# Performance work log

Measured on AMD Instinct MI355X. Metric: run time of the kernel, lower is better.

Reference implementation:

```python
import jax, jax.numpy as jnp
import numpy as np

H = 32       # num query heads
KV = 8       # num kv heads
HD = 128     # head dim
G = H // KV  # groups


def setup_inputs() -> dict:
    key = jax.random.key(0)
    ks = jax.random.split(key, 7)
    B, S, P, D = 2, 2048, 1024, 4096
    s = 1.0 / np.sqrt(D)
    return {
        "x": jax.random.normal(ks[0], (B, S, D), jnp.float32),
        "past_k": jax.random.normal(ks[1], (B, P, KV, HD), jnp.float32),
        "past_v": jax.random.normal(ks[2], (B, P, KV, HD), jnp.float32),
        "Wq": jax.random.normal(ks[3], (D, H * HD), jnp.float32) * s,
        "Wk": jax.random.normal(ks[4], (D, KV * HD), jnp.float32) * s,
        "Wv": jax.random.normal(ks[5], (D, KV * HD), jnp.float32) * s,
        "Wo": jax.random.normal(ks[6], (D, D), jnp.float32) * s,
    }


def reference(x, past_k, past_v, Wq, Wk, Wv, Wo):
    B, S, D = x.shape
    q = (x @ Wq).reshape(B, S, H, HD)    # [B,S,H,hd]
    k = (x @ Wk).reshape(B, S, KV, HD)
    v = (x @ Wv).reshape(B, S, KV, HD)
    # KV-cache append (cache slice [:, :end])
    k_full = jnp.concatenate([past_k, k], axis=1)  # [B,T,KV,hd]
    v_full = jnp.concatenate([past_v, v], axis=1)
    T = k_full.shape[1]
    # repeat_interleave over head dim -> each kv head serves G query heads
    k_rep = jnp.repeat(k_full, G, axis=2)  # [B,T,H,hd]
    v_rep = jnp.repeat(v_full, G, axis=2)
    scale = 1.0 / np.sqrt(HD)
    scores = jnp.einsum('bshd,bthd->bhst', q, k_rep) * scale  # [B,H,S,T]
    # causal mask with cache offset: query i attends to j <= (T - S) + i
    allowed = (jnp.arange(S)[:, None] + (T - S)) >= jnp.arange(T)[None, :]
    scores = jnp.where(allowed[None, None], scores, jnp.float32(-jnp.inf))
    attn = jax.nn.softmax(scores, axis=-1)
    out = jnp.einsum('bhst,bthd->bshd', attn, v_rep).reshape(B, S, D)
    return out @ Wo
```

## Files before the change

### kernel.cpp

```cpp
#include <hip/hip_runtime.h>

typedef __bf16 bf16x8 __attribute__((ext_vector_type(8)));
typedef float f32x4 __attribute__((ext_vector_type(4)));
using gptr_t = const __attribute__((address_space(1))) void*;
using sptr_t = __attribute__((address_space(3))) void*;

#define B_ 2
#define S_ 2048
#define D_ 4096
#define H_ 32
#define KV_ 8
#define G_ 4
#define HD_ 128
#define P_ 1024
#define T_ 3072

__device__ inline bf16x8 cvt8(const float4 a, const float4 b) {
  bf16x8 r;
  r[0] = (__bf16)a.x; r[1] = (__bf16)a.y; r[2] = (__bf16)a.z; r[3] = (__bf16)a.w;
  r[4] = (__bf16)b.x; r[5] = (__bf16)b.y; r[6] = (__bf16)b.z; r[7] = (__bf16)b.w;
  return r;
}

__global__ __launch_bounds__(256) void cvt_f32_bf16(const float* __restrict__ in,
                                                    __bf16* __restrict__ out) {
  const long i = ((long)blockIdx.x * 256 + threadIdx.x) * 8;
  float4 a = *(const float4*)(in + i);
  float4 b = *(const float4*)(in + i + 4);
  *(bf16x8*)(out + i) = cvt8(a, b);
}

__global__ __launch_bounds__(256) void transpose2d(const float* __restrict__ in,
                                                   __bf16* __restrict__ out,
                                                   int R, int C) {
  __shared__ float tl[32][33];
  const int tx = threadIdx.x, ty = threadIdx.y;
  const int c0 = blockIdx.x * 32, r0 = blockIdx.y * 32;
#pragma unroll
  for (int i = 0; i < 4; ++i)
    tl[ty + i * 8][tx] = in[(long)(r0 + ty + i * 8) * C + c0 + tx];
  __syncthreads();
#pragma unroll
  for (int i = 0; i < 4; ++i)
    out[(long)(c0 + ty + i * 8) * R + r0 + tx] = (__bf16)tl[tx][ty + i * 8];
}

__global__ __launch_bounds__(256) void build_vt(const float* __restrict__ past_v,
                                                const __bf16* __restrict__ vn,
                                                __bf16* __restrict__ vt) {
  __shared__ float tl[32][33];
  const int tx = threadIdx.x, ty = threadIdx.y;
  const int j0 = blockIdx.x * 32, hd0 = blockIdx.y * 32;
  const int b = blockIdx.z >> 3, kvh = blockIdx.z & 7;
#pragma unroll
  for (int i = 0; i < 4; ++i) {
    const int j = j0 + ty + i * 8;
    float val = (j < P_)
        ? past_v[((long)((b * P_ + j) * KV_ + kvh)) * HD_ + hd0 + tx]
        : (float)vn[((long)((b * S_ + (j - P_)) * KV_ + kvh)) * HD_ + hd0 + tx];
    tl[ty + i * 8][tx] = val;
  }
  __syncthreads();
#pragma unroll
  for (int i = 0; i < 4; ++i)
    vt[((long)((b * KV_ + kvh) * HD_ + hd0 + ty + i * 8)) * T_ + j0 + tx] =
        (__bf16)tl[tx][ty + i * 8];
}

template <typename OutT>
__global__ __launch_bounds__(256, 3) void gemm_bt(const __bf16* __restrict__ A,
                                                  const __bf16* __restrict__ Bt,
                                                  OutT* __restrict__ C,
                                                  int M, int N, int K) {
  __shared__ __align__(16) __bf16 As[128][32];
  __shared__ __align__(16) __bf16 Bs[128][32];
  const int t = threadIdx.x;
  const int lane = t & 63, wave = t >> 6;
  const int wm = (wave >> 1) * 64, wn = (wave & 1) * 64;
  const int l15 = lane & 15, quad = lane >> 4;
  const long m0 = (long)blockIdx.y * 128, n0 = (long)blockIdx.x * 128;

  const int srow = wave * 32 + (lane >> 2);
  const int scol = (lane & 3) * 8;
  const __bf16* Ap = A + (m0 + srow) * K + scol;
  const __bf16* Bp = Bt + (n0 + srow) * K + scol;
  const long rstep = 16L * K;
  sptr_t ldsA0 = (sptr_t)&As[wave * 32][0];
  sptr_t ldsA1 = (sptr_t)&As[wave * 32 + 16][0];
  sptr_t ldsB0 = (sptr_t)&Bs[wave * 32][0];
  sptr_t ldsB1 = (sptr_t)&Bs[wave * 32 + 16][0];

  f32x4 acc[4][4];
#pragma unroll
  for (int i = 0; i < 4; ++i)
#pragma unroll
    for (int j = 0; j < 4; ++j)
#pragma unroll
      for (int e = 0; e < 4; ++e) acc[i][j][e] = 0.0f;

  const int nk = K >> 5;
  for (int kt = 0; kt < nk; ++kt) {
    __syncthreads();
    __builtin_amdgcn_global_load_lds((gptr_t)(Ap + kt * 32), ldsA0, 16, 0, 0);
    __builtin_amdgcn_global_load_lds((gptr_t)(Ap + rstep + kt * 32), ldsA1, 16, 0, 0);
    __builtin_amdgcn_global_load_lds((gptr_t)(Bp + kt * 32), ldsB0, 16, 0, 0);
    __builtin_amdgcn_global_load_lds((gptr_t)(Bp + rstep + kt * 32), ldsB1, 16, 0, 0);
    __syncthreads();
    bf16x8 aF[4], bF[4];
#pragma unroll
    for (int i = 0; i < 4; ++i)
      aF[i] = *(const bf16x8*)(&As[wm + i * 16 + l15][quad * 8]);
#pragma unroll
    for (int i = 0; i < 4; ++i)
      bF[i] = *(const bf16x8*)(&Bs[wn + i * 16 + l15][quad * 8]);
#pragma unroll
    for (int i = 0; i < 4; ++i)
#pragma unroll
      for (int j = 0; j < 4; ++j)
        acc[i][j] = __builtin_amdgcn_mfma_f32_16x16x32_bf16(aF[i], bF[j],
                                                            acc[i][j], 0, 0, 0);
  }

#pragma unroll
  for (int i = 0; i < 4; ++i) {
    const long r0 = m0 + wm + i * 16 + quad * 4;
#pragma unroll
    for (int j = 0; j < 4; ++j) {
      const long col = n0 + wn + j * 16 + l15;
#pragma unroll
      for (int r = 0; r < 4; ++r)
        C[(r0 + r) * N + col] = (OutT)acc[i][j][r];
    }
  }
}

__global__ __launch_bounds__(256, 2) void attn_kernel(
    __bf16* qio,
    const float* __restrict__ pk,
    const __bf16* __restrict__ kn,
    const __bf16* __restrict__ vt) {
  __shared__ __align__(16) __bf16 Ks[64][136];
  __shared__ __align__(16) __bf16 Vs[128][72];
  __shared__ __align__(16) __bf16 Ps[4][32][72];
  const int t = threadIdx.x;
  const int lane = t & 63, w = t >> 6;
  const int l15 = lane & 15, quad = lane >> 4;
  const int s0 = blockIdx.x * 128;
  const int h = blockIdx.y, b = blockIdx.z;
  const int kvh = h >> 2;

  bf16x8 aQ[2][4];
#pragma unroll
  for (int mi = 0; mi < 2; ++mi) {
    const int qrow = s0 + w * 32 + mi * 16 + l15;
    const __bf16* qp = qio + ((long)((b * S_ + qrow) * H_ + h)) * HD_ + quad * 8;
#pragma unroll
    for (int kt = 0; kt < 4; ++kt) aQ[mi][kt] = *(const bf16x8*)(qp + kt * 32);
  }

  f32x4 O[2][8];
#pragma unroll
  for (int mi = 0; mi < 2; ++mi)
#pragma unroll
    for (int f = 0; f < 8; ++f)
#pragma unroll
      for (int e = 0; e < 4; ++e) O[mi][f][e] = 0.0f;
  float m_r[2][4], l_r[2][4];
#pragma unroll
  for (int mi = 0; mi < 2; ++mi)
#pragma unroll
    for (int r = 0; r < 4; ++r) { m_r[mi][r] = -__builtin_inff(); l_r[mi][r] = 0.0f; }

  bf16x8 ones;
#pragma unroll
  for (int e = 0; e < 8; ++e) ones[e] = (__bf16)1.0f;

  const float C2 = 1.4426950408889634f * 0.08838834764831845f;
  const int ntiles = (P_ + s0 + 128) / 64;
  const int wave_last_key = P_ + s0 + w * 32 + 31;
  const int wave_min_bound = P_ + s0 + w * 32;

  for (int tile = 0; tile < ntiles; ++tile) {
    const int j0 = tile * 64;
    __syncthreads();
#pragma unroll
    for (int p = 0; p < 4; ++p) {
      const int li = p * 256 + t;
      const int key = li >> 4, ch = (li & 15) * 8;
      const int j = j0 + key;
      bf16x8 kv;
      if (j < P_) {
        const float* src = pk + ((long)((b * P_ + j) * KV_ + kvh)) * HD_ + ch;
        kv = cvt8(*(const float4*)src, *(const float4*)(src + 4));
      } else {
        kv = *(const bf16x8*)(kn + ((long)((b * S_ + (j - P_)) * KV_ + kvh)) * HD_ + ch);
      }
      *(bf16x8*)(&Ks[key][ch]) = kv;
    }
#pragma unroll
    for (int p = 0; p < 4; ++p) {
      const int li = p * 256 + t;
      const int hd = li >> 3, k8 = (li & 7) * 8;
      *(bf16x8*)(&Vs[hd][k8]) =
          *(const bf16x8*)(vt + ((long)((b * KV_ + kvh) * HD_ + hd)) * T_ + j0 + k8);
    }
    __syncthreads();

    if (j0 > wave_last_key) continue;

    f32x4 sc[2][4];
#pragma unroll
    for (int mi = 0; mi < 2; ++mi)
#pragma unroll
      for (int kf = 0; kf < 4; ++kf)
#pragma unroll
        for (int e = 0; e < 4; ++e) sc[mi][kf][e] = 0.0f;
#pragma unroll
    for (int kf = 0; kf < 4; ++kf) {
#pragma unroll
      for (int kt = 0; kt < 4; ++kt) {
        bf16x8 bk = *(const bf16x8*)(&Ks[kf * 16 + l15][kt * 32 + quad * 8]);
        sc[0][kf] = __builtin_amdgcn_mfma_f32_16x16x32_bf16(aQ[0][kt], bk, sc[0][kf], 0, 0, 0);
        sc[1][kf] = __builtin_amdgcn_mfma_f32_16x16x32_bf16(aQ[1][kt], bk, sc[1][kf], 0, 0, 0);
      }
    }

    const bool need_mask = (j0 + 63 > wave_min_bound);
    float alpha[2][4];
#pragma unroll
    for (int mi = 0; mi < 2; ++mi) {
#pragma unroll
      for (int r = 0; r < 4; ++r) {
        float v0 = sc[mi][0][r], v1 = sc[mi][1][r];
        float v2 = sc[mi][2][r], v3 = sc[mi][3][r];
        if (need_mask) {
          const int bound = P_ + s0 + w * 32 + mi * 16 + quad * 4 + r;
          v0 = (j0 + l15 <= bound) ? v0 : -__builtin_inff();
          v1 = (j0 + 16 + l15 <= bound) ? v1 : -__builtin_inff();
          v2 = (j0 + 32 + l15 <= bound) ? v2 : -__builtin_inff();
          v3 = (j0 + 48 + l15 <= bound) ? v3 : -__builtin_inff();
        }
        float mt = fmaxf(fmaxf(v0, v1), fmaxf(v2, v3));
        mt = fmaxf(mt, __shfl_xor(mt, 1));
        mt = fmaxf(mt, __shfl_xor(mt, 2));
        mt = fmaxf(mt, __shfl_xor(mt, 4));
        mt = fmaxf(mt, __shfl_xor(mt, 8));
        const float mn = fmaxf(m_r[mi][r], mt);
        const float p0 = exp2f((v0 - mn) * C2);
        const float p1 = exp2f((v1 - mn) * C2);
        const float p2 = exp2f((v2 - mn) * C2);
        const float p3 = exp2f((v3 - mn) * C2);
        alpha[mi][r] = exp2f((m_r[mi][r] - mn) * C2);
        m_r[mi][r] = mn;
        const int row = mi * 16 + quad * 4 + r;
        Ps[w][row][l15] = (__bf16)p0;
        Ps[w][row][16 + l15] = (__bf16)p1;
        Ps[w][row][32 + l15] = (__bf16)p2;
        Ps[w][row][48 + l15] = (__bf16)p3;
      }
    }
#pragma unroll
    for (int mi = 0; mi < 2; ++mi)
#pragma unroll
      for (int f = 0; f < 8; ++f)
#pragma unroll
        for (int r = 0; r < 4; ++r) O[mi][f][r] *= alpha[mi][r];

    f32x4 sums[2];
#pragma unroll
    for (int e = 0; e < 4; ++e) { sums[0][e] = 0.0f; sums[1][e] = 0.0f; }
#pragma unroll
    for (int kf2 = 0; kf2 < 2; ++kf2) {
      bf16x8 aP0 = *(const bf16x8*)(&Ps[w][l15][kf2 * 32 + quad * 8]);
      bf16x8 aP1 = *(const bf16x8*)(&Ps[w][16 + l15][kf2 * 32 + quad * 8]);
      sums[0] = __builtin_amdgcn_mfma_f32_16x16x32_bf16(aP0, ones, sums[0], 0, 0, 0);
      sums[1] = __builtin_amdgcn_mfma_f32_16x16x32_bf16(aP1, ones, sums[1], 0, 0, 0);
#pragma unroll
      for (int f = 0; f < 8; ++f) {
        bf16x8 bV = *(const bf16x8*)(&Vs[f * 16 + l15][kf2 * 32 + quad * 8]);
        O[0][f] = __builtin_amdgcn_mfma_f32_16x16x32_bf16(aP0, bV, O[0][f], 0, 0, 0);
        O[1][f] = __builtin_amdgcn_mfma_f32_16x16x32_bf16(aP1, bV, O[1][f], 0, 0, 0);
      }
    }
#pragma unroll
    for (int mi = 0; mi < 2; ++mi)
#pragma unroll
      for (int r = 0; r < 4; ++r)
        l_r[mi][r] = l_r[mi][r] * alpha[mi][r] + sums[mi][r];
  }

#pragma unroll
  for (int mi = 0; mi < 2; ++mi) {
#pragma unroll
    for (int r = 0; r < 4; ++r) {
      const float inv = 1.0f / l_r[mi][r];
      const long row =
          (long)((b * S_ + s0 + w * 32 + mi * 16 + quad * 4 + r) * H_ + h);
#pragma unroll
      for (int f = 0; f < 8; ++f)
        qio[row * HD_ + f * 16 + l15] = (__bf16)(O[mi][f][r] * inv);
    }
  }
}

extern "C" void kernel_launch(void* const* d_in, const int* in_sizes, int n_in,
                              void* d_out, int out_size, void* d_ws, size_t ws_size,
                              hipStream_t stream) {
  const float* x  = (const float*)d_in[0];
  const float* pk = (const float*)d_in[1];
  const float* pv = (const float*)d_in[2];
  const float* Wq = (const float*)d_in[3];
  const float* Wk = (const float*)d_in[4];
  const float* Wv = (const float*)d_in[5];
  const float* Wo = (const float*)d_in[6];
  float* out = (float*)d_out;
  char* ws = (char*)d_ws;
  __bf16* wt = (__bf16*)(ws);
  __bf16* q  = (__bf16*)(ws + (size_t)33554432);
  __bf16* kn = (__bf16*)(ws + (size_t)67108864);
  __bf16* vn = (__bf16*)(ws + (size_t)75497472);
  __bf16* xb = (__bf16*)(ws + (size_t)83886080);
  __bf16* vt = (__bf16*)(ws + (size_t)83886080);

  dim3 tb(32, 8);
  cvt_f32_bf16<<<8192, 256, 0, stream>>>(x, xb);
  transpose2d<<<dim3(128, 128), tb, 0, stream>>>(Wq, wt, D_, D_);
  gemm_bt<__bf16><<<dim3(32, 32), 256, 0, stream>>>(xb, wt, q, B_ * S_, D_, D_);
  transpose2d<<<dim3(32, 128), tb, 0, stream>>>(Wk, wt, D_, KV_ * HD_);
  gemm_bt<__bf16><<<dim3(8, 32), 256, 0, stream>>>(xb, wt, kn, B_ * S_, KV_ * HD_, D_);
  transpose2d<<<dim3(32, 128), tb, 0, stream>>>(Wv, wt, D_, KV_ * HD_);
  gemm_bt<__bf16><<<dim3(8, 32), 256, 0, stream>>>(xb, wt, vn, B_ * S_, KV_ * HD_, D_);
  build_vt<<<dim3(96, 4, 16), tb, 0, stream>>>(pv, vn, vt);
  attn_kernel<<<dim3(16, 32, 2), 256, 0, stream>>>(q, pk, kn, vt);
  transpose2d<<<dim3(128, 128), tb, 0, stream>>>(Wo, wt, D_, D_);
  gemm_bt<float><<<dim3(32, 32), 256, 0, stream>>>(q, wt, out, B_ * S_, D_, D_);
}
```

Before: 1.219 ms.

## Fuse K/V projections, prebuild bf16 K cache, async LDS loads with swizzle

Fuses the K and V projection GEMMs into a single N=2048 GEMM and adds a pre-pass that builds a contiguous bf16 K cache per (batch, kv-head), so the attention kernel no longer converts fp32 past_k on the fly. The attention kernel now loads K and V tiles directly global-to-LDS with global_load_lds using an XOR-swizzled layout instead of padded arrays. It also reorders the grid so the longest causal query blocks are scheduled first, and raises the occupancy hint to 3. The costs are an extra build kernel and more workspace traffic, plus the risk that the swizzle addressing is wrong.

New measurement: 1.436 ms. 17.8% more time.

```diff
diff --git a/kernel.cpp b/kernel.cpp
--- a/kernel.cpp
+++ b/kernel.cpp
@@ -45,8 +45,27 @@
     out[(long)(c0 + ty + i * 8) * R + r0 + tx] = (__bf16)tl[tx][ty + i * 8];
 }
 
+__global__ __launch_bounds__(256) void build_kc(const float* __restrict__ pk,
+                                                const __bf16* __restrict__ kv,
+                                                __bf16* __restrict__ kc) {
+  const int i = blockIdx.x * 256 + threadIdx.x;
+  const int hd0 = (i & 15) * 8;
+  const int row = i >> 4;
+  const int j = row % T_;
+  const int bk = row / T_;
+  const int b = bk >> 3, kvh = bk & 7;
+  bf16x8 v;
+  if (j < P_) {
+    const float* src = pk + ((long)((b * P_ + j) * KV_ + kvh)) * HD_ + hd0;
+    v = cvt8(*(const float4*)src, *(const float4*)(src + 4));
+  } else {
+    v = *(const bf16x8*)(kv + (long)(b * S_ + (j - P_)) * 2048 + kvh * HD_ + hd0);
+  }
+  *(bf16x8*)(kc + (long)row * HD_ + hd0) = v;
+}
+
 __global__ __launch_bounds__(256) void build_vt(const float* __restrict__ past_v,
-                                                const __bf16* __restrict__ vn,
+                                                const __bf16* __restrict__ kv,
                                                 __bf16* __restrict__ vt) {
   __shared__ float tl[32][33];
   const int tx = threadIdx.x, ty = threadIdx.y;
@@ -57,7 +76,7 @@
     const int j = j0 + ty + i * 8;
     float val = (j < P_)
         ? past_v[((long)((b * P_ + j) * KV_ + kvh)) * HD_ + hd0 + tx]
-        : (float)vn[((long)((b * S_ + (j - P_)) * KV_ + kvh)) * HD_ + hd0 + tx];
+        : (float)kv[(long)(b * S_ + (j - P_)) * 2048 + 1024 + kvh * HD_ + hd0 + tx];
     tl[ty + i * 8][tx] = val;
   }
   __syncthreads();
@@ -134,19 +153,18 @@
   }
 }
 
-__global__ __launch_bounds__(256, 2) void attn_kernel(
+__global__ __launch_bounds__(256, 3) void attn_kernel(
     __bf16* qio,
-    const float* __restrict__ pk,
-    const __bf16* __restrict__ kn,
+    const __bf16* __restrict__ kc,
     const __bf16* __restrict__ vt) {
-  __shared__ __align__(16) __bf16 Ks[64][136];
-  __shared__ __align__(16) __bf16 Vs[128][72];
+  __shared__ __align__(16) __bf16 Ks[64][128];
+  __shared__ __align__(16) __bf16 Vs[128][64];
   __shared__ __align__(16) __bf16 Ps[4][32][72];
   const int t = threadIdx.x;
   const int lane = t & 63, w = t >> 6;
   const int l15 = lane & 15, quad = lane >> 4;
-  const int s0 = blockIdx.x * 128;
-  const int h = blockIdx.y, b = blockIdx.z;
+  const int s0 = (15 - blockIdx.z) * 128;
+  const int h = blockIdx.x, b = blockIdx.y;
   const int kvh = h >> 2;
 
   bf16x8 aQ[2][4];
@@ -157,6 +175,15 @@
 #pragma unroll
     for (int kt = 0; kt < 4; ++kt) aQ[mi][kt] = *(const bf16x8*)(qp + kt * 32);
   }
+
+  const int l4 = lane >> 4;
+  const int kb = (lane & 15) * 16;
+  const int koff_e = l4 * 256 + (kb ^ (l4 << 4));
+  const int koff_o = l4 * 256 + (kb ^ ((4 + l4) << 4));
+  const int vrow = lane >> 3;
+  const int vboff = ((lane & 7) * 16) ^ (vrow << 4);
+  const __bf16* kc_h = kc + (long)(b * KV_ + kvh) * T_ * HD_;
+  const __bf16* vt_h = vt + (long)((b * KV_ + kvh) * HD_) * T_;
 
   f32x4 O[2][8];
 #pragma unroll
@@ -180,29 +207,30 @@
   const int wave_last_key = P_ + s0 + w * 32 + 31;
   const int wave_min_bound = P_ + s0 + w * 32;
 
+  const int sw = (l15 & 7) << 4;
+  const char* KsB = (const char*)&Ks[0][0];
+  const char* VsB = (const char*)&Vs[0][0];
+
   for (int tile = 0; tile < ntiles; ++tile) {
     const int j0 = tile * 64;
     __syncthreads();
-#pragma unroll
-    for (int p = 0; p < 4; ++p) {
-      const int li = p * 256 + t;
-      const int key = li >> 4, ch = (li & 15) * 8;
-      const int j = j0 + key;
-      bf16x8 kv;
-      if (j < P_) {
-        const float* src = pk + ((long)((b * P_ + j) * KV_ + kvh)) * HD_ + ch;
-        kv = cvt8(*(const float4*)src, *(const float4*)(src + 4));
-      } else {
-        kv = *(const bf16x8*)(kn + ((long)((b * S_ + (j - P_)) * KV_ + kvh)) * HD_ + ch);
-      }
-      *(bf16x8*)(&Ks[key][ch]) = kv;
-    }
-#pragma unroll
-    for (int p = 0; p < 4; ++p) {
-      const int li = p * 256 + t;
-      const int hd = li >> 3, k8 = (li & 7) * 8;
-      *(bf16x8*)(&Vs[hd][k8]) =
-          *(const bf16x8*)(vt + ((long)((b * KV_ + kvh) * HD_ + hd)) * T_ + j0 + k8);
+    {
+      const char* kbase = (const char*)(kc_h + (long)j0 * HD_);
+      const char* vbase = (const char*)vt_h + (long)j0 * 2;
+#pragma unroll
+      for (int c = 0; c < 4; ++c) {
+        const int i = w * 4 + c;
+        __builtin_amdgcn_global_load_lds(
+            (gptr_t)(kbase + i * 1024 + ((c & 1) ? koff_o : koff_e)),
+            (sptr_t)((char*)&Ks[0][0] + i * 1024), 16, 0, 0);
+      }
+#pragma unroll
+      for (int c = 0; c < 4; ++c) {
+        const int i = w * 4 + c;
+        __builtin_amdgcn_global_load_lds(
+            (gptr_t)(vbase + (long)(i * 8 + vrow) * (T_ * 2) + vboff),
+            (sptr_t)((char*)&Vs[0][0] + i * 1024), 16, 0, 0);
+      }
     }
     __syncthreads();
 
@@ -219,7 +247,8 @@
     for (int kf = 0; kf < 4; ++kf) {
 #pragma unroll
       for (int kt = 0; kt < 4; ++kt) {
-        bf16x8 bk = *(const bf16x8*)(&Ks[kf * 16 + l15][kt * 32 + quad * 8]);
+        bf16x8 bk = *(const bf16x8*)(
+            KsB + ((((kf * 16 + l15) << 8) + kt * 64 + quad * 16) ^ sw));
         sc[0][kf] = __builtin_amdgcn_mfma_f32_16x16x32_bf16(aQ[0][kt], bk, sc[0][kf], 0, 0, 0);
         sc[1][kf] = __builtin_amdgcn_mfma_f32_16x16x32_bf16(aQ[1][kt], bk, sc[1][kf], 0, 0, 0);
       }
@@ -277,7 +306,8 @@
       sums[1] = __builtin_amdgcn_mfma_f32_16x16x32_bf16(aP1, ones, sums[1], 0, 0, 0);
 #pragma unroll
       for (int f = 0; f < 8; ++f) {
-        bf16x8 bV = *(const bf16x8*)(&Vs[f * 16 + l15][kf2 * 32 + quad * 8]);
+        bf16x8 bV = *(const bf16x8*)(
+            VsB + ((((f * 16 + l15) << 7) + kf2 * 64 + quad * 16) ^ sw));
         O[0][f] = __builtin_amdgcn_mfma_f32_16x16x32_bf16(aP0, bV, O[0][f], 0, 0, 0);
         O[1][f] = __builtin_amdgcn_mfma_f32_16x16x32_bf16(aP1, bV, O[1][f], 0, 0, 0);
       }
@@ -315,23 +345,23 @@
   const float* Wo = (const float*)d_in[6];
   float* out = (float*)d_out;
   char* ws = (char*)d_ws;
-  __bf16* wt = (__bf16*)(ws);
-  __bf16* q  = (__bf16*)(ws + (size_t)33554432);
-  __bf16* kn = (__bf16*)(ws + (size_t)67108864);
-  __bf16* vn = (__bf16*)(ws + (size_t)75497472);
-  __bf16* xb = (__bf16*)(ws + (size_t)83886080);
-  __bf16* vt = (__bf16*)(ws + (size_t)83886080);
+  __bf16* wt  = (__bf16*)ws;
+  __bf16* kvb = (__bf16*)(ws + (size_t)16777216);
+  __bf16* q   = (__bf16*)(ws + (size_t)33554432);
+  __bf16* xb  = (__bf16*)(ws + (size_t)67108864);
+  __bf16* kc  = (__bf16*)(ws + (size_t)67108864);
+  __bf16* vt  = (__bf16*)(ws + (size_t)79691776);
 
   dim3 tb(32, 8);
   cvt_f32_bf16<<<8192, 256, 0, stream>>>(x, xb);
   transpose2d<<<dim3(128, 128), tb, 0, stream>>>(Wq, wt, D_, D_);
   gemm_bt<__bf16><<<dim3(32, 32), 256, 0, stream>>>(xb, wt, q, B_ * S_, D_, D_);
   transpose2d<<<dim3(32, 128), tb, 0, stream>>>(Wk, wt, D_, KV_ * HD_);
-  gemm_bt<__bf16><<<dim3(8, 32), 256, 0, stream>>>(xb, wt, kn, B_ * S_, KV_ * HD_, D_);
-  transpose2d<<<dim3(32, 128), tb, 0, stream>>>(Wv, wt, D_, KV_ * HD_);
-  gemm_bt<__bf16><<<dim3(8, 32), 256, 0, stream>>>(xb, wt, vn, B_ * S_, KV_ * HD_, D_);
-  build_vt<<<dim3(96, 4, 16), tb, 0, stream>>>(pv, vn, vt);
-  attn_kernel<<<dim3(16, 32, 2), 256, 0, stream>>>(q, pk, kn, vt);
+  transpose2d<<<dim3(32, 128), tb, 0, stream>>>(Wv, wt + (size_t)1024 * 4096, D_, KV_ * HD_);
+  gemm_bt<__bf16><<<dim3(16, 32), 256, 0, stream>>>(xb, wt, kvb, B_ * S_, 2048, D_);
+  build_kc<<<3072, 256, 0, stream>>>(pk, kvb, kc);
+  build_vt<<<dim3(96, 4, 16), tb, 0, stream>>>(pv, kvb, vt);
+  attn_kernel<<<dim3(32, 2, 16), 256, 0, stream>>>(q, kc, vt);
   transpose2d<<<dim3(128, 128), tb, 0, stream>>>(Wo, wt, D_, D_);
   gemm_bt<float><<<dim3(32, 32), 256, 0, stream>>>(q, wt, out, B_ * S_, D_, D_);
 }
```
